# Kernel optimization log

Hardware: AMD Instinct MI355X
Metric: run time of the kernel (lower is better)

## Reference

```python
import jax, jax.numpy as jnp
import numpy as np

S, M, B, D, H, DH = 1024, 1024, 4, 1024, 16, 64
T = S + M
EPS = 1e-5


def setup_inputs() -> dict:
    key = jax.random.key(0)
    ks = jax.random.split(key, 6)
    x = jax.random.normal(ks[0], (S, B, D), dtype=jnp.float32)
    pos_emb = jax.random.normal(ks[1], (S, 1, D), dtype=jnp.float32)
    memory = jax.random.normal(ks[2], (M, B, D), dtype=jnp.float32)
    # causal mask: query i (global position M+i) cannot attend to key j > M+i
    i = jnp.arange(S)[:, None]
    j = jnp.arange(T)[None, :]
    mask = jnp.broadcast_to((j > (i + M))[:, :, None], (S, T, B))  # [S,T,B] bool
    w_qkv = jax.random.normal(ks[3], (D, 3 * H * DH), dtype=jnp.float32) * (D ** -0.5)
    w_o = jax.random.normal(ks[4], (H * DH, D), dtype=jnp.float32) * ((H * DH) ** -0.5)
    ln_gamma = jnp.ones((D,), dtype=jnp.float32)
    ln_beta = jnp.zeros((D,), dtype=jnp.float32)
    return {"x": x, "pos_emb": pos_emb, "memory": memory, "mask": mask,
            "w_qkv": w_qkv, "w_o": w_o, "ln_gamma": ln_gamma, "ln_beta": ln_beta}


def reference(x, pos_emb, memory, mask, w_qkv, w_o, ln_gamma, ln_beta):
    seq_len = x.shape[0]
    scale = 1.0 / (DH ** 0.5)
    x = x + pos_emb[-seq_len:]                      # [S,B,D]
    c = jnp.concatenate([memory, x], axis=0)        # [T,B,D]
    qkv = jnp.einsum('tbd,de->tbe', c, w_qkv)       # [T,B,3*H*DH]
    q, k, v = jnp.split(qkv, 3, axis=-1)
    q = q.reshape(-1, B, H, DH)[-seq_len:]          # [S,B,H,DH]
    k = k.reshape(-1, B, H, DH)                     # [T,B,H,DH]
    v = v.reshape(-1, B, H, DH)
    score = jnp.einsum('ibnd,jbnd->ijbn', q, k) * scale  # [S,T,B,H]
    score = jnp.where(mask[:, :, :, None], -jnp.inf, score)
    prob = jax.nn.softmax(score, axis=1)
    vec = jnp.einsum('ijbn,jbnd->ibnd', prob, v)    # [S,B,H,DH]
    vec = vec.reshape(seq_len, B, H * DH)
    attn_out = jnp.einsum('sbe,ed->sbd', vec, w_o)  # [S,B,D]
    y = x + attn_out
    mu = jnp.mean(y, axis=-1, keepdims=True)
    var = jnp.mean(jnp.square(y - mu), axis=-1, keepdims=True)
    out = (y - mu) * jax.lax.rsqrt(var + EPS) * ln_gamma + ln_beta
    return out
```

## Files before the change

### kernel.cpp

```cpp
#include <hip/hip_runtime.h>
#include <stdint.h>

#define S_  1024
#define M_  1024
#define B_  4
#define D_  1024
#define H_  16
#define DH_ 64
#define T_  2048

typedef __attribute__((ext_vector_type(8))) short bf8;
typedef __attribute__((ext_vector_type(4))) float f32x4;
typedef __attribute__((ext_vector_type(16))) float f32x16;
typedef __attribute__((ext_vector_type(8))) unsigned short u16x8;
typedef __attribute__((ext_vector_type(4))) unsigned short u16x4;
typedef __attribute__((ext_vector_type(4))) unsigned int u32x4;
typedef unsigned short u16;

#define MFMA(a, b, c)   __builtin_amdgcn_mfma_f32_16x16x32_bf16((a), (b), (c), 0, 0, 0)
#define MFMA32(a, b, c) __builtin_amdgcn_mfma_f32_32x32x16_bf16((a), (b), (c), 0, 0, 0)

#define SIG(r) ((((r) >> 1) ^ ((r) >> 3)) & 3)

static __device__ __forceinline__ u16 f2bf(float f) {
  unsigned int u = __builtin_bit_cast(unsigned int, f);
  u += 0x7fffu + ((u >> 16) & 1u);
  return (u16)(u >> 16);
}

static __device__ __forceinline__ void gload16(const void* g, void* l) {
  __builtin_amdgcn_global_load_lds((const __attribute__((address_space(1))) unsigned int*)g,
                                   (__attribute__((address_space(3))) unsigned int*)l,
                                   16, 0, 0);
}

static __device__ __forceinline__ float fexp2(float x) {
  return __builtin_amdgcn_exp2f(x);
}
static __device__ __forceinline__ unsigned int cvtpk(float lo, float hi) {
  unsigned int r; asm("v_cvt_pk_bf16_f32 %0, %1, %2" : "=v"(r) : "v"(lo), "v"(hi)); return r;
}
static __device__ __forceinline__ void plswap(unsigned int& a, unsigned int& b) {
  asm volatile("s_nop 1\n\tv_permlane32_swap_b32 %0, %1" : "+v"(a), "+v"(b));
}

__global__ __launch_bounds__(256) void k_prep(const float* __restrict__ x,
    const float* __restrict__ pos, const float* __restrict__ mem,
    u16* __restrict__ cbf, float* __restrict__ xp)
{
  const int gid = blockIdx.x * 256 + threadIdx.x;
  const int e = gid * 8;
  const int row = e >> 10, col = e & 1023;
  float4 v0, v1;
  if (e < M_ * B_ * D_) {
    v0 = *(const float4*)(mem + e);
    v1 = *(const float4*)(mem + e + 4);
  } else {
    const int i2 = e - M_ * B_ * D_;
    v0 = *(const float4*)(x + i2);
    v1 = *(const float4*)(x + i2 + 4);
    const int srow = i2 >> 12;
    const float4 p0 = *(const float4*)(pos + srow * 1024 + col);
    const float4 p1 = *(const float4*)(pos + srow * 1024 + col + 4);
    v0.x += p0.x; v0.y += p0.y; v0.z += p0.z; v0.w += p0.w;
    v1.x += p1.x; v1.y += p1.y; v1.z += p1.z; v1.w += p1.w;
    *(float4*)(xp + i2) = v0;
    *(float4*)(xp + i2 + 4) = v1;
  }
  u16x8 c;
  c[0] = f2bf(v0.x); c[1] = f2bf(v0.y); c[2] = f2bf(v0.z); c[3] = f2bf(v0.w);
  c[4] = f2bf(v1.x); c[5] = f2bf(v1.y); c[6] = f2bf(v1.z); c[7] = f2bf(v1.w);
  const int ch = col >> 3;
  const int chs = (ch & ~3) | ((ch & 3) ^ SIG(row));
  *(u16x8*)(cbf + (size_t)row * 1024 + chs * 8) = c;
}

__global__ __launch_bounds__(256) void k_wtrans(const float* __restrict__ src,
    u16* __restrict__ dst, int Rr, int Cc, int swz)
{
  __shared__ float tl[64][65];
  const int r0 = blockIdx.x * 64, c0 = blockIdx.y * 64;
  const int tid = threadIdx.x;
  const int lr = tid >> 4, lc = (tid & 15) * 4;
  for (int i = 0; i < 4; ++i) {
    const int rr = lr + i * 16;
    const float4 v = *(const float4*)(src + (size_t)(r0 + rr) * Cc + c0 + lc);
    tl[rr][lc] = v.x; tl[rr][lc + 1] = v.y; tl[rr][lc + 2] = v.z; tl[rr][lc + 3] = v.w;
  }
  __syncthreads();
  const int c = tid >> 2, k0 = (tid & 3) * 16;
  u16x8 a, b;
  for (int j = 0; j < 8; ++j) { a[j] = f2bf(tl[k0 + j][c]); b[j] = f2bf(tl[k0 + 8 + j][c]); }
  const int roww = c0 + c;
  int ch0 = (r0 + k0) >> 3, ch1 = ((r0 + k0) >> 3) + 1;
  if (swz) {
    const int sx = SIG(roww);
    ch0 = (ch0 & ~3) | ((ch0 & 3) ^ sx);
    ch1 = (ch1 & ~3) | ((ch1 & 3) ^ sx);
  }
  u16* dp = dst + (size_t)roww * Rr;
  *(u16x8*)(dp + ch0 * 8) = a;
  *(u16x8*)(dp + ch1 * 8) = b;
}

__global__ __launch_bounds__(256, 3) void k_gemm_qkvs(const u16* __restrict__ A,
    const u16* __restrict__ Bt, u16* __restrict__ Qd, u16* __restrict__ Kd,
    u16* __restrict__ VTd)
{
  __shared__ u16 sA[3][4096];
  __shared__ u16 sB[3][4096];
  const int tid = threadIdx.x, lane = tid & 63, wave = tid >> 6;
  const int lrow = lane & 15, lgrp = lane >> 4;
  const int wm = (wave >> 1) * 64, wn = (wave & 1) * 64;
  const int sr = lane >> 2, sk = (lane & 3) * 8;

  const int bid = blockIdx.x;
  const int lid = (bid & 7) * 160 + (bid >> 3);
  int rowb, colb;
  if (lid < 512) { rowb = lid >> 4; colb = 8 + (lid & 15); }
  else { const int l2 = lid - 512; const int q = l2 / 24; rowb = 32 + q; colb = l2 - q * 24; }
  const int row0 = rowb * 128, col0 = colb * 128;

  f32x4 acc[4][4];
#pragma unroll
  for (int i = 0; i < 4; ++i)
#pragma unroll
    for (int j = 0; j < 4; ++j) acc[i][j] = f32x4{0.f, 0.f, 0.f, 0.f};

#define STAGE_S(bufi, kt) do { const int k0_ = (kt) * 32;                      \
    _Pragma("unroll") for (int s_ = 0; s_ < 2; ++s_) {                         \
      const int rr_ = (wave * 2 + s_) * 16 + sr;                               \
      gload16(A + (size_t)(row0 + rr_) * 1024 + k0_ + sk,                      \
              &sA[bufi][(wave * 2 + s_) * 512]);                               \
      gload16(Bt + (size_t)(col0 + rr_) * 1024 + k0_ + sk,                     \
              &sB[bufi][(wave * 2 + s_) * 512]);                               \
    } } while (0)

  STAGE_S(0, 0); STAGE_S(1, 1);

  int c0 = 0;
#pragma unroll 1
  for (int t = 0; t < 32; ++t) {
    if (t < 31) { asm volatile("s_waitcnt vmcnt(4)" ::: "memory"); }
    else        { asm volatile("s_waitcnt vmcnt(0)" ::: "memory"); }
    __builtin_amdgcn_s_barrier();
    __builtin_amdgcn_sched_barrier(0);
    const int c2 = (c0 + 2 >= 3) ? c0 - 1 : c0 + 2;
    if (t <= 29) STAGE_S(c2, t + 2);
    bf8 af[4], bfv[4];
#pragma unroll
    for (int i = 0; i < 4; ++i) {
      const int r_ = wm + i * 16 + lrow;
      af[i] = *(const bf8*)&sA[c0][r_ * 32 + ((lgrp ^ SIG(r_)) << 3)];
    }
#pragma unroll
    for (int j = 0; j < 4; ++j) {
      const int r_ = wn + j * 16 + lrow;
      bfv[j] = *(const bf8*)&sB[c0][r_ * 32 + ((lgrp ^ SIG(r_)) << 3)];
    }
    __builtin_amdgcn_s_setprio(1);
#pragma unroll
    for (int i = 0; i < 4; ++i)
#pragma unroll
      for (int j = 0; j < 4; ++j) acc[i][j] = MFMA(af[i], bfv[j], acc[i][j]);
    __builtin_amdgcn_s_setprio(0);
    c0 = (c0 == 2) ? 0 : c0 + 1;
  }

  const int which = col0 >> 10;
#pragma unroll
  for (int i = 0; i < 4; ++i)
#pragma unroll
    for (int j = 0; j < 4; ++j)
#pragma unroll
      for (int r = 0; r < 4; ++r) {
        const int grow = row0 + wm + i * 16 + lgrp * 4 + r;
        const int gcol = col0 + wn + j * 16 + lrow;
        const u16 bv = f2bf(acc[i][j][r]);
        const int t = grow >> 2, bb2 = grow & 3;
        const int rem = gcol & 1023;
        const int bh = bb2 * 16 + (rem >> 6), dh = rem & 63;
        if (which == 0) {
          if (t >= M_) Qd[((size_t)bh * S_ + (t - M_)) * 64 + dh] = bv;
        } else if (which == 1) {
          Kd[((size_t)bh * T_ + t) * 64 + (dh ^ ((t & 7) << 3))] = bv;
        } else {
          VTd[((size_t)bh * 64 + dh) * T_ + (t & ~63) + ((t & 63) ^ ((dh & 7) << 3))] = bv;
        }
      }
}

__global__ __launch_bounds__(256) void k_gemm_out(const u16* __restrict__ A,
    const u16* __restrict__ Bt, const float* __restrict__ xp,
    float* __restrict__ y)
{
  __shared__ u16 sA[2][2048];
  __shared__ u16 sB[2][4096];
  const int tid = threadIdx.x, lane = tid & 63, wave = tid >> 6;
  const int lrow = lane & 15, lgrp = lane >> 4;
  const int wm = (wave >> 1) * 32, wn = (wave & 1) * 64;
  const int row0 = blockIdx.y * 64, col0 = blockIdx.x * 128;
  const int sr = lane >> 2, sk = (lane & 3) * 8;

  f32x4 acc[2][4];
  for (int i = 0; i < 2; ++i)
    for (int j = 0; j < 4; ++j) acc[i][j] = f32x4{0.f, 0.f, 0.f, 0.f};

#define STAGE_O(buf, kt) do { const int k0_ = (kt) * 32;                       \
    const int rra_ = wave * 16 + sr;                                           \
    gload16(A + (size_t)(row0 + rra_) * 1024 + k0_ + sk,                       \
            &sA[buf][wave * 512]);                                             \
    for (int s_ = 0; s_ < 2; ++s_) {                                           \
      const int rrb_ = (wave * 2 + s_) * 16 + sr;                              \
      gload16(Bt + (size_t)(col0 + rrb_) * 1024 + k0_ + sk,                    \
              &sB[buf][(wave * 2 + s_) * 512]);                                \
    } } while (0)

  STAGE_O(0, 0);
  int cur = 0;
  for (int kt = 0; kt < 32; ++kt) {
    asm volatile("s_waitcnt vmcnt(0)" ::: "memory");
    __syncthreads();
    if (kt + 1 < 32) STAGE_O(cur ^ 1, kt + 1);
    bf8 af[2], bfv[4];
    const u16* pa = &sA[cur][(wm + lrow) * 32 + lgrp * 8];
    const u16* pb = &sB[cur][(wn + lrow) * 32 + lgrp * 8];
    for (int i = 0; i < 2; ++i) af[i] = *(const bf8*)(pa + i * 512);
    for (int j = 0; j < 4; ++j) bfv[j] = *(const bf8*)(pb + j * 512);
    __builtin_amdgcn_s_setprio(1);
    for (int i = 0; i < 2; ++i)
      for (int j = 0; j < 4; ++j) acc[i][j] = MFMA(af[i], bfv[j], acc[i][j]);
    __builtin_amdgcn_s_setprio(0);
    cur ^= 1;
  }

  for (int i = 0; i < 2; ++i)
    for (int j = 0; j < 4; ++j)
      for (int r = 0; r < 4; ++r) {
        const int grow = row0 + wm + i * 16 + lgrp * 4 + r;
        const int gcol = col0 + wn + j * 16 + lrow;
        y[(size_t)grow * 1024 + gcol] = acc[i][j][r] + xp[(size_t)grow * 1024 + gcol];
      }
}

__global__ __launch_bounds__(256) void k_attn(const u16* __restrict__ Qd,
    const u16* __restrict__ Kd, const u16* __restrict__ VTd,
    u16* __restrict__ vec)
{
  __shared__ u16 Kl[2][4096];
  __shared__ u16 Vl[2][4096];
  const int tid = threadIdx.x, lane = tid & 63, wave = tid >> 6;
  const int ql = lane & 31, hi = lane >> 5;
  const int qb = blockIdx.x, bh = blockIdx.y;
  const int bb = bh >> 4, hh = bh & 15;
  const int q0 = qb * 128 + wave * 32;
  const int myq = q0 + ql;
  const int klim = M_ + myq;

  bf8 qf[4];
  const u16* qrow = Qd + ((size_t)bh * S_ + myq) * 64 + hi * 8;
#pragma unroll
  for (int c = 0; c < 4; ++c) qf[c] = *(const bf8*)(qrow + c * 16);

  const u16* kb = Kd + (size_t)bh * T_ * 64;
  const u16* vb = VTd + (size_t)bh * 64 * T_;

  f32x16 o0, o1;
#pragma unroll
  for (int r = 0; r < 16; ++r) { o0[r] = 0.f; o1[r] = 0.f; }
  float m_run = 0.f, l_run = 0.f;
  const float cs = 0.125f * 1.44269504f;

  const int nkt = (M_ + qb * 128 + 128) >> 6;

  auto stage = [&](int buf, int kt) {
    const int t0 = kt * 64;
#pragma unroll
    for (int i = 0; i < 2; ++i) {
      const int ch = i * 256 + tid;
      gload16(kb + (size_t)t0 * 64 + ch * 8, &Kl[buf][ch * 8]);
    }
#pragma unroll
    for (int i = 0; i < 2; ++i) {
      const int ch = i * 256 + tid;
      gload16(vb + (size_t)(ch >> 3) * T_ + t0 + (ch & 7) * 8, &Vl[buf][ch * 8]);
    }
  };

  stage(0, 0);
  int cur = 0;
  for (int kt = 0; kt < nkt; ++kt) {
    if (kt + 1 < nkt) {
      stage(cur ^ 1, kt + 1);
      asm volatile("s_waitcnt vmcnt(4)" ::: "memory");
    } else {
      asm volatile("s_waitcnt vmcnt(0)" ::: "memory");
    }
    __builtin_amdgcn_s_barrier();

    const u16* Kc = Kl[cur];
    const u16* Vc = Vl[cur];

    f32x16 s0, s1;
#pragma unroll
    for (int r = 0; r < 16; ++r) { s0[r] = 0.f; s1[r] = 0.f; }
    const int tr0 = ql, tr1 = 32 + ql;
    const int sw0 = (tr0 & 7) << 3;
    __builtin_amdgcn_s_setprio(1);
#pragma unroll
    for (int c = 0; c < 4; ++c) {
      const int db = c * 16 + hi * 8;
      const bf8 ka = *(const bf8*)(Kc + tr0 * 64 + (db ^ sw0));
      const bf8 kbfr = *(const bf8*)(Kc + tr1 * 64 + (db ^ sw0));
      s0 = MFMA32(ka, qf[c], s0);
      s1 = MFMA32(kbfr, qf[c], s1);
    }
    __builtin_amdgcn_s_setprio(0);

    float p0[16], p1[16];
#pragma unroll
    for (int r = 0; r < 16; ++r) { p0[r] = s0[r] * cs; p1[r] = s1[r] * cs; }
    if (kt * 64 + 63 > M_ + q0) {
#pragma unroll
      for (int r = 0; r < 16; ++r) {
        const int kg = kt * 64 + (r & 3) + 8 * (r >> 2) + 4 * hi;
        if (kg > klim)      p0[r] = -1e30f;
        if (kg + 32 > klim) p1[r] = -1e30f;
      }
    }
    float mx = fmaxf(p0[0], p1[0]);
#pragma unroll
    for (int r = 1; r < 16; ++r) mx = fmaxf(mx, fmaxf(p0[r], p1[r]));
    mx = fmaxf(mx, __shfl_xor(mx, 32));
    if (__any(mx - m_run > 8.f)) {
      const float mnew = fmaxf(m_run, mx);
      const float al = fexp2(m_run - mnew);
      l_run *= al;
#pragma unroll
      for (int r = 0; r < 16; ++r) {
        const int qloc = (r & 3) + 8 * (r >> 2) + 4 * hi;
        const float ar = __shfl(al, (lane & 32) + qloc);
        o0[r] *= ar; o1[r] *= ar;
      }
      m_run = mnew;
    }
    float rs = 0.f;
#pragma unroll
    for (int r = 0; r < 16; ++r) {
      p0[r] = fexp2(p0[r] - m_run);
      p1[r] = fexp2(p1[r] - m_run);
      rs += p0[r] + p1[r];
    }
    rs += __shfl_xor(rs, 32);
    l_run += rs;

    bf8 paf[2][2];
    {
      unsigned int a0 = cvtpk(p0[0], p0[1]),  a1 = cvtpk(p0[2], p0[3]);
      unsigned int a2 = cvtpk(p0[4], p0[5]),  a3 = cvtpk(p0[6], p0[7]);
      unsigned int b0 = cvtpk(p0[8], p0[9]),  b1 = cvtpk(p0[10], p0[11]);
      unsigned int b2 = cvtpk(p0[12], p0[13]), b3 = cvtpk(p0[14], p0[15]);
      plswap(a0, a2); plswap(a1, a3); plswap(b0, b2); plswap(b1, b3);
      u32x4 f0 = {a0, a1, a2, a3}, f1 = {b0, b1, b2, b3};
      paf[0][0] = __builtin_bit_cast(bf8, f0);
      paf[0][1] = __builtin_bit_cast(bf8, f1);
    }
    {
      unsigned int a0 = cvtpk(p1[0], p1[1]),  a1 = cvtpk(p1[2], p1[3]);
      unsigned int a2 = cvtpk(p1[4], p1[5]),  a3 = cvtpk(p1[6], p1[7]);
      unsigned int b0 = cvtpk(p1[8], p1[9]),  b1 = cvtpk(p1[10], p1[11]);
      unsigned int b2 = cvtpk(p1[12], p1[13]), b3 = cvtpk(p1[14], p1[15]);
      plswap(a0, a2); plswap(a1, a3); plswap(b0, b2); plswap(b1, b3);
      u32x4 f0 = {a0, a1, a2, a3}, f1 = {b0, b1, b2, b3};
      paf[1][0] = __builtin_bit_cast(bf8, f0);
      paf[1][1] = __builtin_bit_cast(bf8, f1);
    }

    __builtin_amdgcn_s_setprio(1);
#pragma unroll
    for (int kc = 0; kc < 4; ++kc) {
      const int tb = kc * 16 + hi * 8;
      const bf8 pfrag = paf[kc >> 1][kc & 1];
      const int vr0 = ql, vr1 = 32 + ql;
      const bf8 vf0 = *(const bf8*)(Vc + vr0 * 64 + (tb ^ ((vr0 & 7) << 3)));
      const bf8 vf1 = *(const bf8*)(Vc + vr1 * 64 + (tb ^ ((vr1 & 7) << 3)));
      o0 = MFMA32(pfrag, vf0, o0);
      o1 = MFMA32(pfrag, vf1, o1);
    }
    __builtin_amdgcn_s_setprio(0);
    __builtin_amdgcn_s_barrier();
    cur ^= 1;
  }

  const float linv = 1.0f / l_run;
#pragma unroll
  for (int r = 0; r < 16; ++r) {
    const int qloc = (r & 3) + 8 * (r >> 2) + 4 * hi;
    const float li = __shfl(linv, (lane & 32) + qloc);
    const int srow = q0 + qloc;
    const size_t base = ((size_t)srow * B_ + bb) * 1024 + hh * 64;
    vec[base + ql]      = f2bf(o0[r] * li);
    vec[base + 32 + ql] = f2bf(o1[r] * li);
  }
}

__global__ __launch_bounds__(256) void k_ln(const float* __restrict__ y,
    const float* __restrict__ g, const float* __restrict__ be,
    float* __restrict__ out)
{
  const int row = blockIdx.x, tid = threadIdx.x;
  const float4 v = *(const float4*)(y + (size_t)row * 1024 + tid * 4);
  float s = v.x + v.y + v.z + v.w;
  float ss = v.x * v.x + v.y * v.y + v.z * v.z + v.w * v.w;
  for (int mk = 1; mk < 64; mk <<= 1) { s += __shfl_xor(s, mk); ss += __shfl_xor(ss, mk); }
  __shared__ float red[8];
  if ((tid & 63) == 0) { red[tid >> 6] = s; red[4 + (tid >> 6)] = ss; }
  __syncthreads();
  s = red[0] + red[1] + red[2] + red[3];
  ss = red[4] + red[5] + red[6] + red[7];
  const float mu = s * (1.0f / 1024.0f);
  const float var = ss * (1.0f / 1024.0f) - mu * mu;
  const float rstd = rsqrtf(var + 1e-5f);
  const float4 gg = *(const float4*)(g + tid * 4);
  const float4 bb = *(const float4*)(be + tid * 4);
  float4 o;
  o.x = (v.x - mu) * rstd * gg.x + bb.x;
  o.y = (v.y - mu) * rstd * gg.y + bb.y;
  o.z = (v.z - mu) * rstd * gg.z + bb.z;
  o.w = (v.w - mu) * rstd * gg.w + bb.w;
  *(float4*)(out + (size_t)row * 1024 + tid * 4) = o;
}

extern "C" void kernel_launch(void* const* d_in, const int* in_sizes, int n_in,
                              void* d_out, int out_size, void* d_ws, size_t ws_size,
                              hipStream_t stream)
{
  const float* x     = (const float*)d_in[0];
  const float* pos   = (const float*)d_in[1];
  const float* mem   = (const float*)d_in[2];
  const float* wqkv  = (const float*)d_in[4];
  const float* wo    = (const float*)d_in[5];
  const float* gamma = (const float*)d_in[6];
  const float* beta  = (const float*)d_in[7];
  float* out = (float*)d_out;

  if (ws_size < ((size_t)104 << 20)) return;

  char* ws = (char*)d_ws;
  u16*   cbf = (u16*)(ws + 0);
  float* y   = (float*)(ws + 0);
  float* xp  = (float*)(ws + ((size_t)16 << 20));
  u16*   wqt = (u16*)(ws + ((size_t)32 << 20));
  u16*   wot = (u16*)(ws + ((size_t)38 << 20));
  u16*   Qd  = (u16*)(ws + ((size_t)40 << 20));
  u16*   Kd  = (u16*)(ws + ((size_t)48 << 20));
  u16*   VTd = (u16*)(ws + ((size_t)80 << 20));
  u16*   vec = (u16*)(ws + ((size_t)96 << 20));

  k_prep<<<4096, 256, 0, stream>>>(x, pos, mem, cbf, xp);
  k_wtrans<<<dim3(16, 48), 256, 0, stream>>>(wqkv, wqt, 1024, 3072, 1);
  k_wtrans<<<dim3(16, 16), 256, 0, stream>>>(wo, wot, 1024, 1024, 0);
  k_gemm_qkvs<<<1280, 256, 0, stream>>>(cbf, wqt, Qd, Kd, VTd);
  k_attn<<<dim3(8, 64), 256, 0, stream>>>(Qd, Kd, VTd, vec);
  k_gemm_out<<<dim3(8, 64), 256, 0, stream>>>(vec, wot, xp, y);
  k_ln<<<4096, 256, 0, stream>>>(y, gamma, beta, out);
}
```

Baseline: 199.6 us.

## Triple-buffer out-projection GEMM, merge weight transposes, swizzle attention block order

The out-projection GEMM moves from double to triple buffering. It waits with a partial vmcnt and uses a single barrier per k-step, so loads run two tiles ahead. The two weight-transpose launches are merged into one kernel that dispatches on blockIdx.y, saving one launch. The attention grid is flattened and its block order is remapped so that consecutive blocks take different query tiles of a head, which balances the causal workload across CUs. Together these target launch overhead, load-latency stalls and tail imbalance, at the cost of extra LDS and a more delicate synchronisation scheme.

```diff
diff --git a/kernel.cpp b/kernel.cpp
--- a/kernel.cpp
+++ b/kernel.cpp
@@ -75,11 +75,16 @@
   *(u16x8*)(cbf + (size_t)row * 1024 + chs * 8) = c;
 }
 
-__global__ __launch_bounds__(256) void k_wtrans(const float* __restrict__ src,
-    u16* __restrict__ dst, int Rr, int Cc, int swz)
+__global__ __launch_bounds__(256) void k_wtrans2(const float* __restrict__ wqkv,
+    const float* __restrict__ wo, u16* __restrict__ wqt, u16* __restrict__ wot)
 {
   __shared__ float tl[64][65];
-  const int r0 = blockIdx.x * 64, c0 = blockIdx.y * 64;
+  const int by = blockIdx.y;
+  const float* src; u16* dst; int Cc, swz, c0;
+  if (by < 48) { src = wqkv; dst = wqt; Cc = 3072; swz = 1; c0 = by * 64; }
+  else         { src = wo;   dst = wot; Cc = 1024; swz = 0; c0 = (by - 48) * 64; }
+  const int Rr = 1024;
+  const int r0 = blockIdx.x * 64;
   const int tid = threadIdx.x;
   const int lr = tid >> 4, lc = (tid & 15) * 4;
   for (int i = 0; i < 4; ++i) {
@@ -194,8 +199,8 @@
     const u16* __restrict__ Bt, const float* __restrict__ xp,
     float* __restrict__ y)
 {
-  __shared__ u16 sA[2][2048];
-  __shared__ u16 sB[2][4096];
+  __shared__ u16 sA[3][2048];
+  __shared__ u16 sB[3][4096];
   const int tid = threadIdx.x, lane = tid & 63, wave = tid >> 6;
   const int lrow = lane & 15, lgrp = lane >> 4;
   const int wm = (wave >> 1) * 32, wn = (wave & 1) * 64;
@@ -206,32 +211,41 @@
   for (int i = 0; i < 2; ++i)
     for (int j = 0; j < 4; ++j) acc[i][j] = f32x4{0.f, 0.f, 0.f, 0.f};
 
-#define STAGE_O(buf, kt) do { const int k0_ = (kt) * 32;                       \
+#define STAGE_O(bufi, kt) do { const int k0_ = (kt) * 32;                      \
     const int rra_ = wave * 16 + sr;                                           \
     gload16(A + (size_t)(row0 + rra_) * 1024 + k0_ + sk,                       \
-            &sA[buf][wave * 512]);                                             \
-    for (int s_ = 0; s_ < 2; ++s_) {                                           \
+            &sA[bufi][wave * 512]);                                            \
+    _Pragma("unroll") for (int s_ = 0; s_ < 2; ++s_) {                         \
       const int rrb_ = (wave * 2 + s_) * 16 + sr;                              \
       gload16(Bt + (size_t)(col0 + rrb_) * 1024 + k0_ + sk,                    \
-              &sB[buf][(wave * 2 + s_) * 512]);                                \
+              &sB[bufi][(wave * 2 + s_) * 512]);                               \
     } } while (0)
 
-  STAGE_O(0, 0);
-  int cur = 0;
+  STAGE_O(0, 0); STAGE_O(1, 1);
+
+  int c0 = 0;
+#pragma unroll 1
   for (int kt = 0; kt < 32; ++kt) {
-    asm volatile("s_waitcnt vmcnt(0)" ::: "memory");
-    __syncthreads();
-    if (kt + 1 < 32) STAGE_O(cur ^ 1, kt + 1);
+    if (kt < 31) { asm volatile("s_waitcnt vmcnt(3)" ::: "memory"); }
+    else         { asm volatile("s_waitcnt vmcnt(0)" ::: "memory"); }
+    __builtin_amdgcn_s_barrier();
+    __builtin_amdgcn_sched_barrier(0);
+    const int c2 = (c0 + 2 >= 3) ? c0 - 1 : c0 + 2;
+    if (kt <= 29) STAGE_O(c2, kt + 2);
     bf8 af[2], bfv[4];
-    const u16* pa = &sA[cur][(wm + lrow) * 32 + lgrp * 8];
-    const u16* pb = &sB[cur][(wn + lrow) * 32 + lgrp * 8];
+    const u16* pa = &sA[c0][(wm + lrow) * 32 + lgrp * 8];
+    const u16* pb = &sB[c0][(wn + lrow) * 32 + lgrp * 8];
+#pragma unroll
     for (int i = 0; i < 2; ++i) af[i] = *(const bf8*)(pa + i * 512);
+#pragma unroll
     for (int j = 0; j < 4; ++j) bfv[j] = *(const bf8*)(pb + j * 512);
     __builtin_amdgcn_s_setprio(1);
+#pragma unroll
     for (int i = 0; i < 2; ++i)
+#pragma unroll
       for (int j = 0; j < 4; ++j) acc[i][j] = MFMA(af[i], bfv[j], acc[i][j]);
     __builtin_amdgcn_s_setprio(0);
-    cur ^= 1;
+    c0 = (c0 == 2) ? 0 : c0 + 1;
   }
 
   for (int i = 0; i < 2; ++i)
@@ -251,7 +265,9 @@
   __shared__ u16 Vl[2][4096];
   const int tid = threadIdx.x, lane = tid & 63, wave = tid >> 6;
   const int ql = lane & 31, hi = lane >> 5;
-  const int qb = blockIdx.x, bh = blockIdx.y;
+  const int bid = blockIdx.x;
+  const int sw = (bid & 7) * 64 + (bid >> 3);
+  const int bh = sw >> 3, qb = sw & 7;
   const int bb = bh >> 4, hh = bh & 15;
   const int q0 = qb * 128 + wave * 32;
   const int myq = q0 + ql;
@@ -458,10 +474,9 @@
   u16*   vec = (u16*)(ws + ((size_t)96 << 20));
 
   k_prep<<<4096, 256, 0, stream>>>(x, pos, mem, cbf, xp);
-  k_wtrans<<<dim3(16, 48), 256, 0, stream>>>(wqkv, wqt, 1024, 3072, 1);
-  k_wtrans<<<dim3(16, 16), 256, 0, stream>>>(wo, wot, 1024, 1024, 0);
+  k_wtrans2<<<dim3(16, 64), 256, 0, stream>>>(wqkv, wo, wqt, wot);
   k_gemm_qkvs<<<1280, 256, 0, stream>>>(cbf, wqt, Qd, Kd, VTd);
-  k_attn<<<dim3(8, 64), 256, 0, stream>>>(Qd, Kd, VTd, vec);
+  k_attn<<<512, 256, 0, stream>>>(Qd, Kd, VTd, vec);
   k_gemm_out<<<dim3(8, 64), 256, 0, stream>>>(vec, wot, xp, y);
   k_ln<<<4096, 256, 0, stream>>>(y, gamma, beta, out);
 }
```

Result: faster. 188.3 us (-5.6%).
